# Performance work log

Hardware: AMD Instinct MI355X
Metric: run time of the kernel (lower is better)

## Reference

```python
import jax, jax.numpy as jnp
import numpy as np

N_NODES = 100000
N_EDGES = 1000000
HIDDEN = 64
IN_DIM = 4


def setup_inputs() -> dict:
    key = jax.random.key(0)
    ks = jax.random.split(key, 7)
    x = jax.random.normal(ks[0], (N_NODES, IN_DIM), dtype=jnp.float32)
    edges = jax.random.randint(ks[1], (N_EDGES, 2), 0, N_NODES, dtype=jnp.int32)
    W1 = jax.random.normal(ks[2], (IN_DIM, HIDDEN), dtype=jnp.float32) * 0.5
    b1 = jax.random.normal(ks[3], (HIDDEN,), dtype=jnp.float32) * 0.1
    phases = jax.random.normal(ks[4], (N_EDGES,), dtype=jnp.float32) * 0.1
    Wout = jax.random.normal(ks[5], (HIDDEN, 1), dtype=jnp.float32) * 0.1
    bout = jax.random.normal(ks[6], (1,), dtype=jnp.float32) * 0.1
    return {"x": x, "edges": edges, "W1": W1, "b1": b1,
            "phases": phases, "Wout": Wout, "bout": bout}


def reference(x, edges, W1, b1, phases, Wout, bout):
    # h = lin(x): [N, D]
    h = x @ W1 + b1
    u = edges[:, 0]  # [E]
    v = edges[:, 1]  # [E]
    c = jnp.cos(phases)  # [E]
    s = jnp.sin(phases)  # [E]
    hu = h[u]  # [E, D] gather
    hv = h[v]  # [E, D] gather
    # rot only mixes the first two channels; the rest pass through (eye).
    # msg to v: rot @ h[u] -> [c*h0 - s*h1, s*h0 + c*h1, h2, ...]
    msg_v = jnp.concatenate([
        (c * hu[:, 0] - s * hu[:, 1])[:, None],
        (s * hu[:, 0] + c * hu[:, 1])[:, None],
        hu[:, 2:],
    ], axis=1)
    # msg to u: rot.T @ h[v] -> [c*h0 + s*h1, -s*h0 + c*h1, h2, ...]
    msg_u = jnp.concatenate([
        (c * hv[:, 0] + s * hv[:, 1])[:, None],
        (-s * hv[:, 0] + c * hv[:, 1])[:, None],
        hv[:, 2:],
    ], axis=1)
    diffused = jnp.zeros_like(h).at[v].add(msg_v).at[u].add(msg_u)  # scatter-add
    return (h + diffused) @ Wout + bout  # [N, 1]
```

## Files before the change

kernel.cpp:

```cpp
#include <hip/hip_runtime.h>
#include <hip/hip_fp16.h>

#define N_NODES 100000
#define N_EDGES 1000000
#define HIDDEN 64

#define N_RANGES 5
#define C_RANGE 20000
#define N_SLICES 102
#define PAIRS (N_EDGES / 2)
#define PPB ((PAIRS + N_SLICES - 1) / N_SLICES)
#define A_THREADS 1024

__device__ __forceinline__ void compute_consts(
    const float* __restrict__ W1, const float* __restrict__ b1,
    const float* __restrict__ Wout, const float* __restrict__ bout,
    float* kc, int tid) {
    if (tid < 64) {
        float wj = Wout[tid];
        float p0 = W1[0 * HIDDEN + tid] * wj;
        float p1 = W1[1 * HIDDEN + tid] * wj;
        float p2 = W1[2 * HIDDEN + tid] * wj;
        float p3 = W1[3 * HIDDEN + tid] * wj;
        float pb = b1[tid] * wj;
        #pragma unroll
        for (int off = 32; off > 0; off >>= 1) {
            p0 += __shfl_down(p0, off);
            p1 += __shfl_down(p1, off);
            p2 += __shfl_down(p2, off);
            p3 += __shfl_down(p3, off);
            pb += __shfl_down(pb, off);
        }
        if (tid < 4) {
            kc[5 + tid] = W1[tid * HIDDEN + 0];
            kc[9 + tid] = W1[tid * HIDDEN + 1];
        }
        if (tid == 0) {
            kc[0] = p0; kc[1] = p1; kc[2] = p2; kc[3] = p3; kc[4] = pb;
            kc[13] = b1[0]; kc[14] = b1[1];
            kc[15] = Wout[0]; kc[16] = Wout[1];
            kc[17] = bout[0];
        }
    }
}

__device__ __forceinline__ float contrib(
    float4 xe, float cs, float sn_signed,
    float c0, float c1, float c2, float c3, float cb,
    float a0, float a1, float a2, float a3,
    float g0, float g1, float g2, float g3,
    float b10, float b11, float w0, float w1) {
    float h0 = xe.x * a0 + xe.y * a1 + xe.z * a2 + xe.w * a3 + b10;
    float h1 = xe.x * g0 + xe.y * g1 + xe.z * g2 + xe.w * g3 + b11;
    float d  = xe.x * c0 + xe.y * c1 + xe.z * c2 + xe.w * c3 + cb;
    float a  = h0 * w0 + h1 * w1;
    float b  = h0 * w1 - h1 * w0;
    return cs * a + sn_signed * b + (d - a);
}

__device__ __forceinline__ unsigned pack_half2(float x, float y) {
    __half2 h = __floats2half2_rn(x, y);
    return *(unsigned*)&h;
}

__global__ __launch_bounds__(A_THREADS, 8) void range_kernel(
    const int4* __restrict__ epairs, const float2* __restrict__ ppairs,
    const float4* __restrict__ x4,
    const float* __restrict__ W1, const float* __restrict__ b1,
    const float* __restrict__ Wout, const float* __restrict__ bout,
    __half* __restrict__ part) {
    __shared__ __align__(16) float bins[C_RANGE];
    __shared__ float kc[18];
    const int tid = threadIdx.x;
    const int r = blockIdx.x / N_SLICES;
    const int s = blockIdx.x - r * N_SLICES;

    compute_consts(W1, b1, Wout, bout, kc, tid);
    {
        float4 z = make_float4(0.f, 0.f, 0.f, 0.f);
        float4* b4 = (float4*)bins;
        for (int j = tid; j < C_RANGE / 4; j += A_THREADS) b4[j] = z;
    }
    __syncthreads();

    const float c0 = kc[0], c1 = kc[1], c2 = kc[2], c3 = kc[3], cb = kc[4];
    const float a0 = kc[5], a1 = kc[6], a2 = kc[7], a3 = kc[8];
    const float g0 = kc[9], g1 = kc[10], g2 = kc[11], g3 = kc[12];
    const float b10 = kc[13], b11 = kc[14], w0 = kc[15], w1 = kc[16];

    const int nlo = r * C_RANGE;
    const int pA = s * PPB;
    const int pB = min(pA + PPB, PAIRS);

    #pragma unroll 2
    for (int p = pA + tid; p < pB; p += A_THREADS) {
        int4   ee = epairs[p];
        float2 pp = ppairs[p];

        unsigned jv0 = (unsigned)(ee.y - nlo);
        unsigned ju0 = (unsigned)(ee.x - nlo);
        unsigned jv1 = (unsigned)(ee.w - nlo);
        unsigned ju1 = (unsigned)(ee.z - nlo);
        bool pv0 = jv0 < C_RANGE, pu0 = ju0 < C_RANGE;
        bool pv1 = jv1 < C_RANGE, pu1 = ju1 < C_RANGE;

        float4 xsv0 = x4[pv0 ? ee.x : 0];
        float4 xsu0 = x4[pu0 ? ee.y : 0];
        float4 xsv1 = x4[pv1 ? ee.z : 0];
        float4 xsu1 = x4[pu1 ? ee.w : 0];

        float sn0, cs0, sn1, cs1;
        __sincosf(pp.x, &sn0, &cs0);
        __sincosf(pp.y, &sn1, &cs1);

        float tv0 = contrib(xsv0, cs0,  sn0, c0,c1,c2,c3,cb, a0,a1,a2,a3, g0,g1,g2,g3, b10,b11,w0,w1);
        float tu0 = contrib(xsu0, cs0, -sn0, c0,c1,c2,c3,cb, a0,a1,a2,a3, g0,g1,g2,g3, b10,b11,w0,w1);
        float tv1 = contrib(xsv1, cs1,  sn1, c0,c1,c2,c3,cb, a0,a1,a2,a3, g0,g1,g2,g3, b10,b11,w0,w1);
        float tu1 = contrib(xsu1, cs1, -sn1, c0,c1,c2,c3,cb, a0,a1,a2,a3, g0,g1,g2,g3, b10,b11,w0,w1);

        if (pv0) atomicAdd(&bins[jv0], tv0);
        if (pu0) atomicAdd(&bins[ju0], tu0);
        if (pv1) atomicAdd(&bins[jv1], tv1);
        if (pu1) atomicAdd(&bins[ju1], tu1);
    }
    __syncthreads();

    uint2* __restrict__ d2 = (uint2*)(part + (size_t)blockIdx.x * C_RANGE);
    const float4* b4 = (const float4*)bins;
    for (int j = tid; j < C_RANGE / 4; j += A_THREADS) {
        float4 v = b4[j];
        d2[j] = make_uint2(pack_half2(v.x, v.y), pack_half2(v.z, v.w));
    }
}

__global__ __launch_bounds__(512) void reduce_kernel(
    const float4* __restrict__ x4,
    const float* __restrict__ W1, const float* __restrict__ b1,
    const float* __restrict__ Wout, const float* __restrict__ bout,
    const __half* __restrict__ part, float* __restrict__ out) {
    __shared__ float kc[18];
    compute_consts(W1, b1, Wout, bout, kc, threadIdx.x);
    __syncthreads();
    int i = blockIdx.x * 512 + threadIdx.x;
    if (i >= N_NODES) return;
    int r = i / C_RANGE;
    int j = i - r * C_RANGE;
    const __half* __restrict__ p = part + (size_t)(r * N_SLICES) * C_RANGE + j;
    float sum = 0.0f;
    #pragma unroll 6
    for (int s = 0; s < N_SLICES; s++) sum += __half2float(p[(size_t)s * C_RANGE]);
    float4 xi = x4[i];
    out[i] = sum + xi.x * kc[0] + xi.y * kc[1] + xi.z * kc[2] + xi.w * kc[3]
           + kc[4] + kc[17];
}

__global__ void precompute_kernel(const float* __restrict__ W1,
                                  const float* __restrict__ b1,
                                  const float* __restrict__ Wout,
                                  const float* __restrict__ bout,
                                  float* __restrict__ consts) {
    __shared__ float kc[18];
    compute_consts(W1, b1, Wout, bout, kc, threadIdx.x);
    __syncthreads();
    if (threadIdx.x < 18) consts[threadIdx.x] = kc[threadIdx.x];
}

__global__ void edge_atomic_kernel(const int2* __restrict__ edges,
                                   const float* __restrict__ phases,
                                   const float4* __restrict__ x4,
                                   const float* __restrict__ consts,
                                   float* __restrict__ rep) {
    int e = blockIdx.x * blockDim.x + threadIdx.x;
    if (e >= N_EDGES) return;
    float c0 = consts[0], c1 = consts[1], c2 = consts[2], c3 = consts[3];
    float cb = consts[4];
    float a0 = consts[5], a1 = consts[6], a2 = consts[7], a3 = consts[8];
    float g0 = consts[9], g1 = consts[10], g2 = consts[11], g3 = consts[12];
    float b10 = consts[13], b11 = consts[14], w0 = consts[15], w1 = consts[16];
    int2 ed = edges[e];
    float ph = phases[e];
    float sn, cs;
    __sincosf(ph, &sn, &cs);
    float4 xu = x4[ed.x];
    float4 xv = x4[ed.y];
    atomicAdd(rep + ed.y, contrib(xu, cs,  sn, c0,c1,c2,c3,cb, a0,a1,a2,a3, g0,g1,g2,g3, b10,b11,w0,w1));
    atomicAdd(rep + ed.x, contrib(xv, cs, -sn, c0,c1,c2,c3,cb, a0,a1,a2,a3, g0,g1,g2,g3, b10,b11,w0,w1));
}

__global__ void final_kernel(const float4* __restrict__ x4,
                             const float* __restrict__ consts,
                             const float* __restrict__ rep,
                             float* __restrict__ out) {
    int i = blockIdx.x * blockDim.x + threadIdx.x;
    if (i >= N_NODES) return;
    float4 xi = x4[i];
    out[i] = rep[i] + xi.x * consts[0] + xi.y * consts[1] + xi.z * consts[2]
           + xi.w * consts[3] + consts[4] + consts[17];
}

extern "C" void kernel_launch(void* const* d_in, const int* in_sizes, int n_in,
                              void* d_out, int out_size, void* d_ws, size_t ws_size,
                              hipStream_t stream) {
    const float* x      = (const float*)d_in[0];
    const int*   edges  = (const int*)d_in[1];
    const float* W1     = (const float*)d_in[2];
    const float* b1     = (const float*)d_in[3];
    const float* phases = (const float*)d_in[4];
    const float* Wout   = (const float*)d_in[5];
    const float* bout   = (const float*)d_in[6];
    float* out = (float*)d_out;

    const size_t part_bytes =
        (size_t)N_RANGES * N_SLICES * C_RANGE * sizeof(__half);

    if (ws_size >= part_bytes) {
        __half* part = (__half*)d_ws;
        range_kernel<<<N_RANGES * N_SLICES, A_THREADS, 0, stream>>>(
            (const int4*)edges, (const float2*)phases, (const float4*)x,
            W1, b1, Wout, bout, part);
        reduce_kernel<<<(N_NODES + 511) / 512, 512, 0, stream>>>(
            (const float4*)x, W1, b1, Wout, bout, part, out);
    } else {
        float* consts = (float*)d_ws;
        float* rep    = (float*)((char*)d_ws + 256);
        hipMemsetAsync(rep, 0, N_NODES * sizeof(float), stream);
        precompute_kernel<<<1, 64, 0, stream>>>(W1, b1, Wout, bout, consts);
        edge_atomic_kernel<<<(N_EDGES + 255) / 256, 256, 0, stream>>>(
            (const int2*)edges, phases, (const float4*)x, consts, rep);
        final_kernel<<<(N_NODES + 255) / 256, 256, 0, stream>>>(
            (const float4*)x, consts, rep, out);
    }
}
```

Baseline: 102.0 us.

## Use fewer, larger node ranges and vectorize reduction over half2 pairs

Shrinks the number of node ranges from 5 to 3, which enlarges each block's shared-memory bin array to about 133 KB. Fewer ranges means each edge pair is rescanned by fewer blocks, and the partial-sum buffer gets smaller. The reduce kernel now has each thread handle two nodes, reading half2 values and writing a float2. The larger LDS footprint limits residency to about one block per CU, which could reduce latency hiding during the atomic-heavy scatter, and the occupancy hint was dropped to match. The last range is partly padded past N_NODES.

```diff
diff --git a/kernel.cpp b/kernel.cpp
--- a/kernel.cpp
+++ b/kernel.cpp
@@ -5,12 +5,13 @@
 #define N_EDGES 1000000
 #define HIDDEN 64
 
-#define N_RANGES 5
-#define C_RANGE 20000
-#define N_SLICES 102
+#define N_RANGES 3
+#define C_RANGE 33344
+#define N_SLICES 85
 #define PAIRS (N_EDGES / 2)
 #define PPB ((PAIRS + N_SLICES - 1) / N_SLICES)
 #define A_THREADS 1024
+#define R_THREADS 256
 
 __device__ __forceinline__ void compute_consts(
     const float* __restrict__ W1, const float* __restrict__ b1,
@@ -63,7 +64,7 @@
     return *(unsigned*)&h;
 }
 
-__global__ __launch_bounds__(A_THREADS, 8) void range_kernel(
+__global__ __launch_bounds__(A_THREADS) void range_kernel(
     const int4* __restrict__ epairs, const float2* __restrict__ ppairs,
     const float4* __restrict__ x4,
     const float* __restrict__ W1, const float* __restrict__ b1,
@@ -133,25 +134,33 @@
     }
 }
 
-__global__ __launch_bounds__(512) void reduce_kernel(
+__global__ __launch_bounds__(R_THREADS) void reduce_kernel(
     const float4* __restrict__ x4,
     const float* __restrict__ W1, const float* __restrict__ b1,
     const float* __restrict__ Wout, const float* __restrict__ bout,
-    const __half* __restrict__ part, float* __restrict__ out) {
+    const __half2* __restrict__ part2, float2* __restrict__ out2) {
     __shared__ float kc[18];
     compute_consts(W1, b1, Wout, bout, kc, threadIdx.x);
     __syncthreads();
-    int i = blockIdx.x * 512 + threadIdx.x;
-    if (i >= N_NODES) return;
-    int r = i / C_RANGE;
-    int j = i - r * C_RANGE;
-    const __half* __restrict__ p = part + (size_t)(r * N_SLICES) * C_RANGE + j;
-    float sum = 0.0f;
-    #pragma unroll 6
-    for (int s = 0; s < N_SLICES; s++) sum += __half2float(p[(size_t)s * C_RANGE]);
-    float4 xi = x4[i];
-    out[i] = sum + xi.x * kc[0] + xi.y * kc[1] + xi.z * kc[2] + xi.w * kc[3]
-           + kc[4] + kc[17];
+    int t = blockIdx.x * R_THREADS + threadIdx.x;
+    int i0 = t * 2;
+    if (i0 >= N_NODES) return;
+    int r = i0 / C_RANGE;
+    int j = i0 - r * C_RANGE;
+    const __half2* __restrict__ p = part2
+        + (size_t)(r * N_SLICES) * (C_RANGE / 2) + (j >> 1);
+    float s0 = 0.0f, s1 = 0.0f;
+    #pragma unroll 5
+    for (int s = 0; s < N_SLICES; s++) {
+        float2 v = __half22float2(p[(size_t)s * (C_RANGE / 2)]);
+        s0 += v.x; s1 += v.y;
+    }
+    float4 xa = x4[i0];
+    float4 xb = x4[i0 + 1];
+    float base = kc[4] + kc[17];
+    out2[t] = make_float2(
+        s0 + xa.x * kc[0] + xa.y * kc[1] + xa.z * kc[2] + xa.w * kc[3] + base,
+        s1 + xb.x * kc[0] + xb.y * kc[1] + xb.z * kc[2] + xb.w * kc[3] + base);
 }
 
 __global__ void precompute_kernel(const float* __restrict__ W1,
@@ -218,8 +227,9 @@
         range_kernel<<<N_RANGES * N_SLICES, A_THREADS, 0, stream>>>(
             (const int4*)edges, (const float2*)phases, (const float4*)x,
             W1, b1, Wout, bout, part);
-        reduce_kernel<<<(N_NODES + 511) / 512, 512, 0, stream>>>(
-            (const float4*)x, W1, b1, Wout, bout, part, out);
+        reduce_kernel<<<(N_NODES / 2 + R_THREADS - 1) / R_THREADS, R_THREADS, 0, stream>>>(
+            (const float4*)x, W1, b1, Wout, bout,
+            (const __half2*)part, (float2*)out);
     } else {
         float* consts = (float*)d_ws;
         float* rep    = (float*)((char*)d_ws + 256);
```

Result: faster. 99.52 us (-2.4%).
